# Performance work log

Measured on AMD Instinct MI355X. Metric: run time of the kernel, lower is better.

The kernel has to match this reference:

```python
import jax, jax.numpy as jnp
import numpy as np
from jax import lax

T, B, I, H = 512, 64, 1024, 1024
MIN_VAL, MAX_VAL = -1.0, 1.0  # ConstScalarClamp bounds for both hardtanh norm-scales


def setup_inputs() -> dict:
    key = jax.random.key(0)
    ks = jax.random.split(key, 12)
    return {
        "inputs": jax.random.normal(ks[0], (T, B, I), jnp.float32),
        "state": jax.random.normal(ks[1], (B, H), jnp.float32),
        "weight_ri": jax.random.normal(ks[2], (H, I), jnp.float32) * 0.02,
        "weight_ii": jax.random.normal(ks[3], (H, I), jnp.float32) * 0.02,
        "weight_ni": jax.random.normal(ks[4], (H, I), jnp.float32) * 0.02,
        "weight_rh": jax.random.normal(ks[5], (H, H), jnp.float32) * 0.02,
        "weight_ih": jax.random.normal(ks[6], (H, H), jnp.float32) * 0.02,
        "weight_nh": jax.random.normal(ks[7], (H, H), jnp.float32) * 0.02,
        "bias_r": jax.random.normal(ks[8], (H,), jnp.float32) * 0.02,
        "bias_i": jax.random.normal(ks[9], (H,), jnp.float32) * 0.02,
        "bias_ni": jax.random.normal(ks[10], (H,), jnp.float32) * 0.02,
        "bias_nh": jax.random.normal(ks[11], (H,), jnp.float32) * 0.02,
    }


def _clamp(x):
    return jnp.clip(x, MIN_VAL, MAX_VAL)


def reference(inputs, state, weight_ri, weight_ii, weight_ni,
              weight_rh, weight_ih, weight_nh,
              bias_r, bias_i, bias_ni, bias_nh):
    # FP quant type: weight proxies are identity, quant_sigmoid/tanh are plain
    # sigmoid/tanh, and both norm-scale QuantHardTanh ops are clamp to [-1, 1].
    h0 = _clamp(state)  # state = norm_scale_out(state) before the loop

    def step(h, x_t):
        x = _clamp(x_t)  # input_quant = norm_scale_out(inputs[i])
        rgate = jax.nn.sigmoid(x @ weight_ri.T + h @ weight_rh.T + bias_r)
        igate = jax.nn.sigmoid(x @ weight_ii.T + h @ weight_ih.T + bias_i)
        gates_ni = x @ weight_ni.T + bias_ni
        gates_nh = h @ weight_nh.T + bias_nh
        ngate = jnp.tanh(_clamp(gates_ni) + _clamp(rgate * gates_nh))
        s = _clamp(h) - ngate
        hy = ngate + _clamp(igate * s)
        return hy, hy

    last, outputs = lax.scan(step, h0, inputs)
    return outputs, last
```

## Files before the change

### kernel.cpp

```cpp
#include <hip/hip_runtime.h>
#include <hip/hip_bf16.h>
#include <cstdio>


typedef short bf16x8 __attribute__((ext_vector_type(8)));
typedef float f32x4 __attribute__((ext_vector_type(4)));
typedef int i32x4 __attribute__((ext_vector_type(4)));

#define NT 512
#define NB 64
#define NH 1024
#define NBH 65536

#define OFF_HBUF  4096UL
#define OFF_WCAT  (OFF_HBUF + 2UL * NB * NH * 4)
#define OFF_WH    (OFF_WCAT + 3UL * NH * NH * 2)
#define OFF_GR    (OFF_WH   + 3UL * NH * NH * 2)
#define OFF_GI    (OFF_GR   + (unsigned long)NT * NB * NH * 2)
#define WS_NEED   (OFF_GI   + (unsigned long)NT * NB * NH * 2)

__device__ __forceinline__ float clampf(float x) { return fminf(fmaxf(x, -1.f), 1.f); }

__device__ __forceinline__ unsigned short f2bf(float x) {
  __hip_bfloat16 h = __float2bfloat16(x);
  union { __hip_bfloat16 h; unsigned short u; } cv;
  cv.h = h;
  return cv.u;
}
__device__ __forceinline__ float bf2f(unsigned short u) {
  return __uint_as_float(((unsigned)u) << 16);
}
__device__ __forceinline__ float frcp(float x) { return __builtin_amdgcn_rcpf(x); }
__device__ __forceinline__ float fsigmoid(float x) { return frcp(1.f + __expf(-x)); }
__device__ __forceinline__ float ftanh(float z) { return 1.f - 2.f * frcp(1.f + __expf(2.f * z)); }

__device__ __forceinline__ i32x4 pack8(float4 v0, float4 v1) {
  i32x4 q;
  q[0] = (int)(f2bf(clampf(v0.x)) | ((unsigned)f2bf(clampf(v0.y)) << 16));
  q[1] = (int)(f2bf(clampf(v0.z)) | ((unsigned)f2bf(clampf(v0.w)) << 16));
  q[2] = (int)(f2bf(clampf(v1.x)) | ((unsigned)f2bf(clampf(v1.y)) << 16));
  q[3] = (int)(f2bf(clampf(v1.z)) | ((unsigned)f2bf(clampf(v1.w)) << 16));
  return q;
}

__device__ __forceinline__ void gload_lds16(const void* g, void* l) {
  __builtin_amdgcn_global_load_lds(
      (const __attribute__((address_space(1))) void*)g,
      (__attribute__((address_space(3))) void*)l, 16, 0, 0);
}

__device__ __forceinline__ void load_frags8(const unsigned short* p, i32x4 a[8]) {
  asm volatile(
      "global_load_dwordx4 %0, %8, off\n\t"
      "global_load_dwordx4 %1, %8, off offset:64\n\t"
      "global_load_dwordx4 %2, %8, off offset:128\n\t"
      "global_load_dwordx4 %3, %8, off offset:192\n\t"
      "global_load_dwordx4 %4, %8, off offset:256\n\t"
      "global_load_dwordx4 %5, %8, off offset:320\n\t"
      "global_load_dwordx4 %6, %8, off offset:384\n\t"
      "global_load_dwordx4 %7, %8, off offset:448\n\t"
      "s_waitcnt vmcnt(0)"
      : "=&v"(a[0]), "=&v"(a[1]), "=&v"(a[2]), "=&v"(a[3]),
        "=&v"(a[4]), "=&v"(a[5]), "=&v"(a[6]), "=&v"(a[7])
      : "v"(p)
      : "memory");
}
__device__ __forceinline__ void store_u32_wt(unsigned int* p, unsigned v) {
  asm volatile("global_store_dword %0, %1, off sc0 sc1" :: "v"(p), "v"(v) : "memory");
}

__global__ void k_convert_weights(const float* __restrict__ wri, const float* __restrict__ wii,
                                  const float* __restrict__ wni, const float* __restrict__ wrh,
                                  const float* __restrict__ wih, const float* __restrict__ wnh,
                                  unsigned short* __restrict__ wcat, unsigned short* __restrict__ wh) {
  const long total = 6L * 1024 * 1024;
  long stride = (long)gridDim.x * blockDim.x * 4;
  for (long i = ((long)blockIdx.x * blockDim.x + threadIdx.x) * 4; i < total; i += stride) {
    int m = (int)(i >> 20);
    long off = i & 1048575L;
    const float* srcs[6] = {wri, wii, wni, wrh, wih, wnh};
    float4 v = *(const float4*)(srcs[m] + off);
    ushort4 o;
    o.x = f2bf(v.x); o.y = f2bf(v.y); o.z = f2bf(v.z); o.w = f2bf(v.w);
    unsigned short* dst = (m < 3) ? (wcat + ((long)m << 20) + off)
                                  : (wh + ((long)(m - 3) << 20) + off);
    *(ushort4*)dst = o;
  }
}

#define BK 64
__launch_bounds__(256)
__global__ void k_gemm_x(const float* __restrict__ A,
                         const unsigned short* __restrict__ Bw,
                         unsigned short* __restrict__ gr, unsigned short* __restrict__ gi,
                         float* __restrict__ gni,
                         const float* __restrict__ br, const float* __restrict__ bi,
                         const float* __restrict__ bni) {
  __shared__ unsigned short As[128 * BK];
  __shared__ unsigned short Bs[128 * BK];

  int bid = blockIdx.x;
  int bm = bid / 24, bn = bid % 24;
  int tid = threadIdx.x;
  int lane = tid & 63, w = tid >> 6;
  int wm = w >> 1, wn = w & 1;

  long arow0 = (long)bm * 128;
  long brow0 = (long)bn * 128;

  f32x4 acc[4][4] = {};

  for (int kt = 0; kt < 1024; kt += BK) {
    __syncthreads();
#pragma unroll
    for (int it = 0; it < 4; ++it) {
      int f = it * 2048 + tid * 8;
      int r = f >> 6, c = f & 63;
      gload_lds16(Bw + (brow0 + r) * 1024 + kt + c, &Bs[f]);
      const float* ap = A + (arow0 + r) * 1024 + kt + c;
      float4 v0 = *(const float4*)ap;
      float4 v1 = *(const float4*)(ap + 4);
      *(i32x4*)(&As[f]) = pack8(v0, v1);
    }
    __syncthreads();
#pragma unroll
    for (int ks = 0; ks < 2; ++ks) {
      bf16x8 a[4], b[4];
#pragma unroll
      for (int fm = 0; fm < 4; ++fm)
        a[fm] = *(const bf16x8*)(&As[(wm * 64 + fm * 16 + (lane & 15)) * BK + ks * 32 + (lane >> 4) * 8]);
#pragma unroll
      for (int fn = 0; fn < 4; ++fn)
        b[fn] = *(const bf16x8*)(&Bs[(wn * 64 + fn * 16 + (lane & 15)) * BK + ks * 32 + (lane >> 4) * 8]);
#pragma unroll
      for (int fm = 0; fm < 4; ++fm)
#pragma unroll
        for (int fn = 0; fn < 4; ++fn)
          acc[fm][fn] = __builtin_amdgcn_mfma_f32_16x16x32_bf16(a[fm], b[fn], acc[fm][fn], 0, 0, 0);
    }
  }

  int g = bn >> 3;
  const float* bias = (g == 0) ? br : (g == 1) ? bi : bni;
#pragma unroll
  for (int fm = 0; fm < 4; ++fm) {
    long m = arow0 + wm * 64 + fm * 16 + (lane >> 4) * 4;
#pragma unroll
    for (int fn = 0; fn < 4; ++fn) {
      long n = brow0 + wn * 64 + fn * 16 + (lane & 15);
      long colg = n & 1023;
      float bv = bias[colg];
#pragma unroll
      for (int r2 = 0; r2 < 4; ++r2) {
        float v = acc[fm][fn][r2] + bv;
        long idx = (m + r2) * 1024 + colg;
        if (g == 0)      gr[idx] = f2bf(v);
        else if (g == 1) gi[idx] = f2bf(v);
        else             gni[idx] = clampf(v);
      }
    }
  }
}

__launch_bounds__(256, 1)
__global__ void k_recurrent(const unsigned short* __restrict__ wh,
                            const unsigned short* __restrict__ gr,
                            const unsigned short* __restrict__ gi,
                            const float* __restrict__ state,
                            const float* __restrict__ bias_nh,
                            unsigned int* __restrict__ hbuf,
                            float* __restrict__ out) {
  __shared__ unsigned short h_lds[8 * 1024];
  __shared__ float red[2][4][3][2][8][16];

  int tid = threadIdx.x;
  int lane = tid & 63, w = tid >> 6;
  int wg = blockIdx.x;
  int grp = wg >> 5;
  int slot = wg & 31;

  int klane = (lane >> 4) * 8;
  int k0 = w * 256;
  i32x4 wfi[3][2][8];
#pragma unroll
  for (int g2 = 0; g2 < 3; ++g2)
#pragma unroll
    for (int n2 = 0; n2 < 2; ++n2) {
      int col = slot * 32 + n2 * 16 + (lane & 15);
      load_frags8(wh + ((long)g2 << 20) + (long)col * 1024 + k0 + klane, wfi[g2][n2]);
    }

  int row = tid >> 5, col = tid & 31;
  long cellofs = (long)(grp * 8 + row) * 1024 + slot * 32 + col;
  float h_local = clampf(state[cellofs]);
  float bnh = bias_nh[slot * 32 + col];

#pragma unroll
  for (int c = 0; c < 8; ++c) {
    const float* sp = state + (long)(grp * 8 + c) * 1024 + k0 + lane * 4;
    float4 v = *(const float4*)sp;
    int2 pv;
    pv.x = (int)(f2bf(clampf(v.x)) | ((unsigned)f2bf(clampf(v.y)) << 16));
    pv.y = (int)(f2bf(clampf(v.z)) | ((unsigned)f2bf(clampf(v.w)) << 16));
    int flat = c * 2048 + (k0 + lane * 4) * 2;
    *(int2*)((char*)h_lds + (flat ^ (c << 4))) = pv;
  }

  const int rowb = (lane & 7) * 2048;
  const int colb = w * 512 + ((lane >> 4) * 16);
  const int rsw = (lane & 7) << 4;

  float grv = bf2f(gr[cellofs]);
  float giv = bf2f(gi[cellofs]);
  float gniv = out[cellofs];

  __syncthreads();

#pragma unroll 1
  for (int t = 0; t < NT; ++t) {
    int par = t & 1;
    f32x4 acc[3][2] = {};
#pragma unroll
    for (int s = 0; s < 8; ++s) {
      bf16x8 a = *(const bf16x8*)((const char*)h_lds + rowb + ((colb + s * 64) ^ rsw));
#pragma unroll
      for (int g2 = 0; g2 < 3; ++g2)
#pragma unroll
        for (int n2 = 0; n2 < 2; ++n2)
          acc[g2][n2] = __builtin_amdgcn_mfma_f32_16x16x32_bf16(
              a, __builtin_bit_cast(bf16x8, wfi[g2][n2][s]), acc[g2][n2], 0, 0, 0);
    }

    int rq = lane >> 4;
    if (rq < 2) {
#pragma unroll
      for (int g2 = 0; g2 < 3; ++g2)
#pragma unroll
        for (int n2 = 0; n2 < 2; ++n2)
#pragma unroll
          for (int r = 0; r < 4; ++r)
            red[par][w][g2][n2][rq * 4 + r][lane & 15] = acc[g2][n2][r];
    }
    __syncthreads();

    int n2c = col >> 4, cc = col & 15;
    float pr = red[par][0][0][n2c][row][cc] + red[par][1][0][n2c][row][cc]
             + red[par][2][0][n2c][row][cc] + red[par][3][0][n2c][row][cc];
    float pi = red[par][0][1][n2c][row][cc] + red[par][1][1][n2c][row][cc]
             + red[par][2][1][n2c][row][cc] + red[par][3][1][n2c][row][cc];
    float pn = red[par][0][2][n2c][row][cc] + red[par][1][2][n2c][row][cc]
             + red[par][2][2][n2c][row][cc] + red[par][3][2][n2c][row][cc];

    float rg = fsigmoid(pr + grv);
    float ig = fsigmoid(pi + giv);
    float ng = ftanh(gniv + clampf(rg * (pn + bnh)));
    float sx = clampf(h_local) - ng;
    float hy = ng + clampf(ig * sx);

    unsigned tgt = (unsigned)(t + 1);
    long bank = (long)(tgt & 1) * NBH;
    store_u32_wt(hbuf + bank + cellofs, ((unsigned)f2bf(hy) << 16) | tgt);
    out[(long)t * NBH + cellofs] = hy;
    h_local = hy;

    if (t + 1 < NT) {
      long g2ofs = (long)tgt * NBH + cellofs;
      grv = bf2f(gr[g2ofs]); giv = bf2f(gi[g2ofs]); gniv = out[g2ofs];

      const unsigned int* base = hbuf + bank + (long)grp * 8192 + k0 + lane * 4;
      i32x4 d[8];
      unsigned done = 0;
      for (unsigned it2 = 0;; ++it2) {
#pragma unroll
        for (int c = 0; c < 8; ++c)
          if (!((done >> c) & 1)) {
            asm volatile("global_load_dwordx4 %0, %1, off sc0 sc1"
                         : "=v"(d[c]) : "v"(base + c * 1024) : "memory");
          }
        asm volatile("s_waitcnt vmcnt(0)" ::: "memory");
#pragma unroll
        for (int c = 0; c < 8; ++c)
          if (!((done >> c) & 1)) {
            unsigned m0 = min((unsigned)d[c][0] & 0xFFFFu, (unsigned)d[c][1] & 0xFFFFu);
            unsigned m1 = min((unsigned)d[c][2] & 0xFFFFu, (unsigned)d[c][3] & 0xFFFFu);
            if (min(m0, m1) >= tgt) done |= (1u << c);
          }
        if (__all((int)(done == 0xFFu)) || it2 > 8192u) break;
        __builtin_amdgcn_s_sleep(1);
      }
#pragma unroll
      for (int c = 0; c < 8; ++c) {
        int flat = c * 2048 + (k0 + lane * 4) * 2;
        int2 v;
        v.x = (int)__builtin_amdgcn_perm((unsigned)d[c][1], (unsigned)d[c][0], 0x07060302u);
        v.y = (int)__builtin_amdgcn_perm((unsigned)d[c][3], (unsigned)d[c][2], 0x07060302u);
        *(int2*)((char*)h_lds + (flat ^ (c << 4))) = v;
      }
    }
  }

  out[(long)NT * NBH + cellofs] = h_local;
}

extern "C" void kernel_launch(void* const* d_in, const int* in_sizes, int n_in,
                              void* d_out, int out_size, void* d_ws, size_t ws_size,
                              hipStream_t stream) {
  const float* inputs = (const float*)d_in[0];
  const float* state  = (const float*)d_in[1];
  const float* wri = (const float*)d_in[2];
  const float* wii = (const float*)d_in[3];
  const float* wni = (const float*)d_in[4];
  const float* wrh = (const float*)d_in[5];
  const float* wih = (const float*)d_in[6];
  const float* wnh = (const float*)d_in[7];
  const float* br  = (const float*)d_in[8];
  const float* bi  = (const float*)d_in[9];
  const float* bni = (const float*)d_in[10];
  const float* bnh = (const float*)d_in[11];

  if (ws_size < WS_NEED) {
    fprintf(stderr, "kernel_launch: ws too small (%zu < %lu)\n", ws_size, WS_NEED);
    return;
  }

  char* ws = (char*)d_ws;
  unsigned int*   hbuf  = (unsigned int*)(ws + OFF_HBUF);
  unsigned short* wcat  = (unsigned short*)(ws + OFF_WCAT);
  unsigned short* whp   = (unsigned short*)(ws + OFF_WH);
  unsigned short* grw   = (unsigned short*)(ws + OFF_GR);
  unsigned short* giw   = (unsigned short*)(ws + OFF_GI);
  float* out = (float*)d_out;

  hipMemsetAsync(ws, 0, OFF_WCAT, stream);
  k_convert_weights<<<512, 256, 0, stream>>>(wri, wii, wni, wrh, wih, wnh, wcat, whp);
  k_gemm_x<<<6144, 256, 0, stream>>>(inputs, wcat, grw, giw, out, br, bi, bni);
  k_recurrent<<<256, 256, 0, stream>>>(whp, grw, giw, state, bnh, hbuf, out);
}
```

Measured before the change: 1.998 ms.

## Halve recurrent workgroup count with 512-thread blocks covering 64 columns each

Restructures the persistent recurrent kernel from 256 workgroups of 256 threads to 128 workgroups of 512 threads, each covering 64 hidden columns using two column halves of four K-split waves. The per-step hidden-state poll is now spread across all 512 threads with a flat coalesced layout and a single min-check, followed by an extra barrier before the next step's LDS reads. Fewer workgroups means fewer pollers on the global handoff buffer and less cross-CU synchronisation traffic. In exchange, each step adds a __syncthreads, and dropping the double-buffered reduction array relies on that barrier for correctness.

```diff
diff --git a/kernel.cpp b/kernel.cpp
--- a/kernel.cpp
+++ b/kernel.cpp
@@ -162,7 +162,7 @@
   }
 }
 
-__launch_bounds__(256, 1)
+__launch_bounds__(512, 1)
 __global__ void k_recurrent(const unsigned short* __restrict__ wh,
                             const unsigned short* __restrict__ gr,
                             const unsigned short* __restrict__ gi,
@@ -171,43 +171,48 @@
                             unsigned int* __restrict__ hbuf,
                             float* __restrict__ out) {
   __shared__ unsigned short h_lds[8 * 1024];
-  __shared__ float red[2][4][3][2][8][16];
+  __shared__ float red[4][3][2][2][8][16];
 
   int tid = threadIdx.x;
   int lane = tid & 63, w = tid >> 6;
+  int ch = w >> 2;
+  int kw = w & 3;
   int wg = blockIdx.x;
-  int grp = wg >> 5;
-  int slot = wg & 31;
+  int grp = wg >> 4;
+  int slot = wg & 15;
 
   int klane = (lane >> 4) * 8;
-  int k0 = w * 256;
+  int k0 = kw * 256;
   i32x4 wfi[3][2][8];
 #pragma unroll
   for (int g2 = 0; g2 < 3; ++g2)
 #pragma unroll
     for (int n2 = 0; n2 < 2; ++n2) {
-      int col = slot * 32 + n2 * 16 + (lane & 15);
+      int col = slot * 64 + ch * 32 + n2 * 16 + (lane & 15);
       load_frags8(wh + ((long)g2 << 20) + (long)col * 1024 + k0 + klane, wfi[g2][n2]);
     }
 
-  int row = tid >> 5, col = tid & 31;
-  long cellofs = (long)(grp * 8 + row) * 1024 + slot * 32 + col;
+  int row = tid >> 6, col = tid & 63;
+  long cellofs = (long)(grp * 8 + row) * 1024 + slot * 64 + col;
   float h_local = clampf(state[cellofs]);
-  float bnh = bias_nh[slot * 32 + col];
-
-#pragma unroll
-  for (int c = 0; c < 8; ++c) {
-    const float* sp = state + (long)(grp * 8 + c) * 1024 + k0 + lane * 4;
+  float bnh = bias_nh[slot * 64 + col];
+
+#pragma unroll
+  for (int c = 0; c < 4; ++c) {
+    int n = c * 512 + tid;
+    int r8 = n >> 8;
+    int coli = (n * 4) & 1023;
+    const float* sp = state + (long)(grp * 8 + r8) * 1024 + coli;
     float4 v = *(const float4*)sp;
     int2 pv;
     pv.x = (int)(f2bf(clampf(v.x)) | ((unsigned)f2bf(clampf(v.y)) << 16));
     pv.y = (int)(f2bf(clampf(v.z)) | ((unsigned)f2bf(clampf(v.w)) << 16));
-    int flat = c * 2048 + (k0 + lane * 4) * 2;
-    *(int2*)((char*)h_lds + (flat ^ (c << 4))) = pv;
+    int flat = n * 8;
+    *(int2*)((char*)h_lds + (flat ^ (r8 << 4))) = pv;
   }
 
   const int rowb = (lane & 7) * 2048;
-  const int colb = w * 512 + ((lane >> 4) * 16);
+  const int colb = kw * 512 + ((lane >> 4) * 16);
   const int rsw = (lane & 7) << 4;
 
   float grv = bf2f(gr[cellofs]);
@@ -218,7 +223,6 @@
 
 #pragma unroll 1
   for (int t = 0; t < NT; ++t) {
-    int par = t & 1;
     f32x4 acc[3][2] = {};
 #pragma unroll
     for (int s = 0; s < 8; ++s) {
@@ -239,17 +243,17 @@
         for (int n2 = 0; n2 < 2; ++n2)
 #pragma unroll
           for (int r = 0; r < 4; ++r)
-            red[par][w][g2][n2][rq * 4 + r][lane & 15] = acc[g2][n2][r];
+            red[kw][g2][n2][ch][rq * 4 + r][lane & 15] = acc[g2][n2][r];
     }
     __syncthreads();
 
-    int n2c = col >> 4, cc = col & 15;
-    float pr = red[par][0][0][n2c][row][cc] + red[par][1][0][n2c][row][cc]
-             + red[par][2][0][n2c][row][cc] + red[par][3][0][n2c][row][cc];
-    float pi = red[par][0][1][n2c][row][cc] + red[par][1][1][n2c][row][cc]
-             + red[par][2][1][n2c][row][cc] + red[par][3][1][n2c][row][cc];
-    float pn = red[par][0][2][n2c][row][cc] + red[par][1][2][n2c][row][cc]
-             + red[par][2][2][n2c][row][cc] + red[par][3][2][n2c][row][cc];
+    int chc = col >> 5, n2c = (col >> 4) & 1, cc = col & 15;
+    float pr = red[0][0][n2c][chc][row][cc] + red[1][0][n2c][chc][row][cc]
+             + red[2][0][n2c][chc][row][cc] + red[3][0][n2c][chc][row][cc];
+    float pi = red[0][1][n2c][chc][row][cc] + red[1][1][n2c][chc][row][cc]
+             + red[2][1][n2c][chc][row][cc] + red[3][1][n2c][chc][row][cc];
+    float pn = red[0][2][n2c][chc][row][cc] + red[1][2][n2c][chc][row][cc]
+             + red[2][2][n2c][chc][row][cc] + red[3][2][n2c][chc][row][cc];
 
     float rg = fsigmoid(pr + grv);
     float ig = fsigmoid(pi + giv);
@@ -267,35 +271,36 @@
       long g2ofs = (long)tgt * NBH + cellofs;
       grv = bf2f(gr[g2ofs]); giv = bf2f(gi[g2ofs]); gniv = out[g2ofs];
 
-      const unsigned int* base = hbuf + bank + (long)grp * 8192 + k0 + lane * 4;
-      i32x4 d[8];
-      unsigned done = 0;
+      const unsigned int* base = hbuf + bank + (long)grp * 8192;
+      i32x4 d[4];
       for (unsigned it2 = 0;; ++it2) {
 #pragma unroll
-        for (int c = 0; c < 8; ++c)
-          if (!((done >> c) & 1)) {
-            asm volatile("global_load_dwordx4 %0, %1, off sc0 sc1"
-                         : "=v"(d[c]) : "v"(base + c * 1024) : "memory");
-          }
+        for (int c = 0; c < 4; ++c) {
+          const unsigned int* p = base + (long)(c * 512 + tid) * 4;
+          asm volatile("global_load_dwordx4 %0, %1, off sc0 sc1"
+                       : "=&v"(d[c]) : "v"(p) : "memory");
+        }
         asm volatile("s_waitcnt vmcnt(0)" ::: "memory");
-#pragma unroll
-        for (int c = 0; c < 8; ++c)
-          if (!((done >> c) & 1)) {
-            unsigned m0 = min((unsigned)d[c][0] & 0xFFFFu, (unsigned)d[c][1] & 0xFFFFu);
-            unsigned m1 = min((unsigned)d[c][2] & 0xFFFFu, (unsigned)d[c][3] & 0xFFFFu);
-            if (min(m0, m1) >= tgt) done |= (1u << c);
-          }
-        if (__all((int)(done == 0xFFu)) || it2 > 8192u) break;
+        unsigned mn = 0xFFFFFFFFu;
+#pragma unroll
+        for (int c = 0; c < 4; ++c)
+#pragma unroll
+          for (int e = 0; e < 4; ++e)
+            mn = min(mn, ((unsigned)d[c][e]) & 0xFFFFu);
+        if (__all((int)(mn >= tgt)) || it2 > 8192u) break;
         __builtin_amdgcn_s_sleep(1);
       }
 #pragma unroll
-      for (int c = 0; c < 8; ++c) {
-        int flat = c * 2048 + (k0 + lane * 4) * 2;
+      for (int c = 0; c < 4; ++c) {
+        int n = c * 512 + tid;
+        int r8 = n >> 8;
+        int flat = n * 8;
         int2 v;
         v.x = (int)__builtin_amdgcn_perm((unsigned)d[c][1], (unsigned)d[c][0], 0x07060302u);
         v.y = (int)__builtin_amdgcn_perm((unsigned)d[c][3], (unsigned)d[c][2], 0x07060302u);
-        *(int2*)((char*)h_lds + (flat ^ (c << 4))) = v;
+        *(int2*)((char*)h_lds + (flat ^ (r8 << 4))) = v;
       }
+      __syncthreads();
     }
   }
 
@@ -334,5 +339,5 @@
   hipMemsetAsync(ws, 0, OFF_WCAT, stream);
   k_convert_weights<<<512, 256, 0, stream>>>(wri, wii, wni, wrh, wih, wnh, wcat, whp);
   k_gemm_x<<<6144, 256, 0, stream>>>(inputs, wcat, grw, giw, out, br, bi, bni);
-  k_recurrent<<<256, 256, 0, stream>>>(whp, grw, giw, state, bnh, hbuf, out);
-}
+  k_recurrent<<<128, 512, 0, stream>>>(whp, grw, giw, state, bnh, hbuf, out);
+}
```

New measurement: 1.757 ms. -12.0%, faster.
